# Kernel optimization log

Measured on AMD Instinct MI355X. Metric: run time of the kernel, lower is better.

## Reference

```python
import jax, jax.numpy as jnp
import numpy as np

N = 100000
NFEAT = 128
NHID = 128
NCLASS = 40
E = 1600000
EPS = 1e-5


def _spmm(vals, src, dst, x, n):
    # y[dst] += vals * x[src]  (sparse adj @ x)
    return jax.ops.segment_sum(vals[:, None] * x[src], dst, num_segments=n)


def _bn(h, gamma, beta, rmean, rvar):
    # BatchNorm1d in eval mode (running statistics)
    return (h - rmean) * jax.lax.rsqrt(rvar + EPS) * gamma + beta


def setup_inputs() -> dict:
    key = jax.random.key(0)
    ks = jax.random.split(key, 24)
    inp = {
        'x': jax.random.normal(ks[0], (N, NFEAT), dtype=jnp.float32),
        'M': jax.random.uniform(ks[1], (N, 1), dtype=jnp.float32),
        'AM': jax.random.uniform(ks[2], (N, 1), dtype=jnp.float32),
        'srcZ': jax.random.randint(ks[3], (E,), 0, N, dtype=jnp.int32),
        'dstZ': jax.random.randint(ks[4], (E,), 0, N, dtype=jnp.int32),
        'valsZ': jax.random.uniform(ks[5], (E,), dtype=jnp.float32),
        'src': jax.random.randint(ks[6], (E,), 0, N, dtype=jnp.int32),
        'dst': jax.random.randint(ks[7], (E,), 0, N, dtype=jnp.int32),
        'vals': jax.random.uniform(ks[8], (E,), dtype=jnp.float32),
        # layer 0 (PaGConv) params
        'W0': jax.random.normal(ks[9], (NHID, NFEAT), dtype=jnp.float32) * (1.414 / np.sqrt(NFEAT)),
        'b0': jnp.zeros((NHID,), dtype=jnp.float32),
        'g0': jnp.ones((NHID,), dtype=jnp.float32),
        'be0': jnp.zeros((NHID,), dtype=jnp.float32),
        'rm0': jax.random.normal(ks[10], (NHID,), dtype=jnp.float32) * 0.1,
        'rv0': jax.random.uniform(ks[11], (NHID,), dtype=jnp.float32) + 0.5,
        # layer 1 (GConv) params
        'W1': jax.random.normal(ks[12], (NHID, NHID), dtype=jnp.float32) * (1.414 / np.sqrt(NHID)),
        'b1': jnp.zeros((NHID,), dtype=jnp.float32),
        'g1': jnp.ones((NHID,), dtype=jnp.float32),
        'be1': jnp.zeros((NHID,), dtype=jnp.float32),
        'rm1': jax.random.normal(ks[13], (NHID,), dtype=jnp.float32) * 0.1,
        'rv1': jax.random.uniform(ks[14], (NHID,), dtype=jnp.float32) + 0.5,
        # layer 2 (GConv) params
        'W2': jax.random.normal(ks[15], (NCLASS, NHID), dtype=jnp.float32) * (1.414 / np.sqrt(NHID)),
        'b2': jnp.zeros((NCLASS,), dtype=jnp.float32),
    }
    return inp


def reference(x, M, AM, srcZ, dstZ, valsZ, src, dst, vals,
              W0, b0, g0, be0, rm0, rv0,
              W1, b1, g1, be1, rm1, rv1,
              W2, b2):
    n = x.shape[0]
    # layer 0: PaGConv with adjZ: fc(spmm(adjZ, M*x) * AM), then BN + ReLU (dropout off in eval)
    h = _spmm(valsZ, srcZ, dstZ, M * x, n) * AM
    h = h @ W0.T + b0
    h = jax.nn.relu(_bn(h, g0, be0, rm0, rv0))
    # layer 1: GConv with adj: fc(spmm(adj, h)), then BN + ReLU
    h = _spmm(vals, src, dst, h, n)
    h = h @ W1.T + b1
    h = jax.nn.relu(_bn(h, g1, be1, rm1, rv1))
    # layer 2: GConv, then log_softmax
    h = _spmm(vals, src, dst, h, n)
    h = h @ W2.T + b2
    return jax.nn.log_softmax(h, axis=-1)
```

## Files before the change

### kernel.cpp

```cpp
#include <hip/hip_runtime.h>
#include <math.h>

#define NFEAT 128
#define NCLS 40
#define NCLSP 64
#define BINROWS 64
#define NBINMAX 1600
#define NBLKC 256
#define CHUNKMAX 6400
#define SEGC 7
#define RSMAX 2048

typedef short bf16x8 __attribute__((ext_vector_type(8)));
typedef float f32x4 __attribute__((ext_vector_type(4)));

__device__ __forceinline__ float bf2f(unsigned int lo16) {
  return __uint_as_float((lo16 & 0xffffu) << 16);
}
__device__ __forceinline__ unsigned int f2bf(float x) {
  unsigned int u = __float_as_uint(x);
  return (u + 0x7fffu + ((u >> 16) & 1u)) >> 16;
}

__global__ __launch_bounds__(256) void prep_misc(
    const float* b0, const float* g0, const float* be0,
    const float* rm0, const float* rv0,
    const float* b1, const float* g1, const float* be1,
    const float* rm1, const float* rv1,
    float* sc0, float* sh0, float* sc1, float* sh1,
    const float* __restrict__ W0, const float* __restrict__ W1,
    const float* __restrict__ W2,
    unsigned short* __restrict__ Wb0, unsigned short* __restrict__ Wb1,
    unsigned short* __restrict__ W2hi, unsigned short* __restrict__ W2lo) {
  int t = threadIdx.x;
  if (blockIdx.x == 0) {
    if (t < 128) {
      float s = g0[t] * rsqrtf(rv0[t] + 1e-5f);
      sc0[t] = s;
      sh0[t] = (b0[t] - rm0[t]) * s + be0[t];
    } else {
      int i = t - 128;
      float s = g1[i] * rsqrtf(rv1[i] + 1e-5f);
      sc1[i] = s;
      sh1[i] = (b1[i] - rm1[i]) * s + be1[i];
    }
    return;
  }
  int i = (blockIdx.x - 1) * 256 + t;
  if (i < 4096) {
    const float* W = (i < 2048) ? W0 : W1;
    unsigned short* Wb = (i < 2048) ? Wb0 : Wb1;
    int j = (i < 2048) ? i : i - 2048;
    const float4* p = (const float4*)(W + (size_t)j * 8);
    float4 v0 = p[0], v1 = p[1];
    unsigned int o0 = f2bf(v0.x) | (f2bf(v0.y) << 16);
    unsigned int o1 = f2bf(v0.z) | (f2bf(v0.w) << 16);
    unsigned int o2 = f2bf(v1.x) | (f2bf(v1.y) << 16);
    unsigned int o3 = f2bf(v1.z) | (f2bf(v1.w) << 16);
    ((uint4*)Wb)[j] = make_uint4(o0, o1, o2, o3);
  } else {
    int j = i - 4096;
    int r = j >> 4;
    float v[8] = {0.f, 0.f, 0.f, 0.f, 0.f, 0.f, 0.f, 0.f};
    if (r < NCLS) {
      const float4* p = (const float4*)(W2 + (size_t)j * 8);
      float4 a = p[0], b = p[1];
      v[0] = a.x; v[1] = a.y; v[2] = a.z; v[3] = a.w;
      v[4] = b.x; v[5] = b.y; v[6] = b.z; v[7] = b.w;
    }
    unsigned int h[8], l[8];
#pragma unroll
    for (int q = 0; q < 8; ++q) {
      h[q] = f2bf(v[q]);
      l[q] = f2bf(v[q] - bf2f(h[q]));
    }
    ((uint4*)W2hi)[j] = make_uint4(h[0] | (h[1] << 16), h[2] | (h[3] << 16),
                                   h[4] | (h[5] << 16), h[6] | (h[7] << 16));
    ((uint4*)W2lo)[j] = make_uint4(l[0] | (l[1] << 16), l[2] | (l[3] << 16),
                                   l[4] | (l[5] << 16), l[6] | (l[7] << 16));
  }
}

__global__ void convert_xm(const float* __restrict__ x, const float* __restrict__ Mv,
                           unsigned short* __restrict__ xm, int n) {
  int i = blockIdx.x * 256 + threadIdx.x;
  if (i >= n * (NFEAT / 8)) return;
  int row = i >> 4;
  float m = Mv[row];
  const float4* p = (const float4*)(x + (size_t)i * 8);
  float4 v0 = p[0], v1 = p[1];
  unsigned int o0 = f2bf(v0.x * m) | (f2bf(v0.y * m) << 16);
  unsigned int o1 = f2bf(v0.z * m) | (f2bf(v0.w * m) << 16);
  unsigned int o2 = f2bf(v1.x * m) | (f2bf(v1.y * m) << 16);
  unsigned int o3 = f2bf(v1.z * m) | (f2bf(v1.w * m) << 16);
  ((uint4*)xm)[i] = make_uint4(o0, o1, o2, o3);
}

__global__ __launch_bounds__(256) void bin_sort2(
    const int* __restrict__ srcZ, const int* __restrict__ dstZ, const float* __restrict__ valZ,
    const int* __restrict__ srcA, const int* __restrict__ dstA, const float* __restrict__ valA,
    int2* __restrict__ DrmZ, int2* __restrict__ DrmA,
    int2* __restrict__ binsCZ, int2* __restrict__ binsCA,
    int E, int nbin, int chunk) {
  __shared__ int2 stage[CHUNKMAX];
  __shared__ int cur[NBINMAX];
  __shared__ int ps[256];
  const int t = threadIdx.x;
  int k = blockIdx.x;
  const int* srcp; const int* dstp; const float* valp; int2* Drm; int2* binsC;
  if (k < NBLKC) {
    srcp = srcZ; dstp = dstZ; valp = valZ; Drm = DrmZ; binsC = binsCZ;
  } else {
    k -= NBLKC;
    srcp = srcA; dstp = dstA; valp = valA; Drm = DrmA; binsC = binsCA;
  }
  for (int i = t; i < nbin; i += 256) cur[i] = 0;
  __syncthreads();
  const int e0 = k * chunk, e1 = min(E, e0 + chunk);
#pragma unroll 4
  for (int e = e0 + t; e < e1; e += 256) atomicAdd(&cur[dstp[e] >> 6], 1);
  __syncthreads();
  int loc[SEGC], cnt[SEGC];
  int s = 0;
#pragma unroll
  for (int j = 0; j < SEGC; ++j) {
    int i = t * SEGC + j;
    int v = (i < nbin) ? cur[i] : 0;
    loc[j] = s; cnt[j] = v;
    s += v;
  }
  ps[t] = s;
  __syncthreads();
  for (int o = 1; o < 256; o <<= 1) {
    int x = (t >= o) ? ps[t - o] : 0;
    __syncthreads();
    ps[t] += x;
    __syncthreads();
  }
  int ex = ps[t] - s;
#pragma unroll
  for (int j = 0; j < SEGC; ++j) {
    int i = t * SEGC + j;
    if (i < nbin) {
      int o = ex + loc[j];
      Drm[(size_t)k * nbin + i] = make_int2(e0 + o, cnt[j]);
      cur[i] = o;
    }
  }
  __syncthreads();
#pragma unroll 2
  for (int e = e0 + t; e < e1; e += 256) {
    int d = dstp[e];
    int p = atomicAdd(&cur[d >> 6], 1);
    stage[p] = make_int2(srcp[e] | ((d & 63) << 17), __float_as_int(valp[e]));
  }
  __syncthreads();
  const int n = e1 - e0;
  for (int i = t; i < n; i += 256) binsC[e0 + i] = stage[i];
}

__global__ __launch_bounds__(256) void transposeD2(
    const int2* __restrict__ DrmZ, const int2* __restrict__ DrmA,
    int2* __restrict__ DbmZ, int2* __restrict__ DbmA,
    int* __restrict__ binTotZ, int* __restrict__ binTotA, int nbin, int tdb) {
  __shared__ int2 st[8][256];
  __shared__ int part[256];
  int t = threadIdx.x;
  int b = blockIdx.x;
  const int2* Drm; int2* Dbm; int* binTot;
  if (b < tdb) {
    Drm = DrmZ; Dbm = DbmZ; binTot = binTotZ;
  } else {
    b -= tdb;
    Drm = DrmA; Dbm = DbmA; binTot = binTotA;
  }
  int i0 = b * 8;
#pragma unroll
  for (int j = 0; j < 8; ++j) {
    int i = i0 + j;
    st[j][t] = (i < nbin) ? Drm[(size_t)t * nbin + i] : make_int2(0, 0);
  }
  __syncthreads();
  {
    int j = t >> 5, ks = (t & 31) * 8;
    int i = i0 + j;
    if (i < nbin) {
      int2* q = &Dbm[(size_t)i * NBLKC + ks];
#pragma unroll
      for (int m = 0; m < 8; ++m) q[m] = st[j][ks + m];
    }
    int p = 0;
#pragma unroll
    for (int m = 0; m < 8; ++m) p += st[j][ks + m].y;
    part[t] = p;
  }
  __syncthreads();
  if (t < 8) {
    int s = 0;
    for (int k = 0; k < 32; ++k) s += part[t * 32 + k];
    if (i0 + t < nbin) binTot[i0 + t] = s;
  }
}

__global__ __launch_bounds__(256) void bin_start2(
    const int* __restrict__ btZ, const int* __restrict__ btA,
    int* __restrict__ bsZ, int* __restrict__ bsA, int nbin) {
  __shared__ int ps[256];
  int t = threadIdx.x;
  const int* bt = (blockIdx.x == 0) ? btZ : btA;
  int* bs = (blockIdx.x == 0) ? bsZ : bsA;
  int C = (nbin + 255) / 256;
  int loc[SEGC + 1];
  int sum = 0;
  for (int j = 0; j < C; ++j) {
    int i = t * C + j;
    loc[j] = sum;
    sum += (i < nbin) ? bt[i] : 0;
  }
  ps[t] = sum;
  __syncthreads();
  for (int o = 1; o < 256; o <<= 1) {
    int x = (t >= o) ? ps[t - o] : 0;
    __syncthreads();
    ps[t] += x;
    __syncthreads();
  }
  int ex = ps[t] - sum;
  for (int j = 0; j < C; ++j) {
    int i = t * C + j;
    if (i < nbin) bs[i] = ex + loc[j];
  }
  if (t == 255) bs[nbin] = ps[255];
}

__global__ __launch_bounds__(256) void row_sort2(
    const int2* __restrict__ DbmZ, const int2* __restrict__ DbmA,
    const int2* __restrict__ binsCZ, const int2* __restrict__ binsCA,
    const int* __restrict__ binStartZ, const int* __restrict__ binStartA,
    int2* __restrict__ bins2Z, int2* __restrict__ bins2A,
    int* __restrict__ rowptrZ, int* __restrict__ rowptrA, int n, int nbin) {
  __shared__ int2 stage[RSMAX];
  __shared__ int ps[256];
  __shared__ int rcnt[BINROWS];
  __shared__ int roff[BINROWS];
  int b = blockIdx.x;
  const int t = threadIdx.x;
  const int2* Dbm; const int2* binsC; const int* binStart; int2* bins2; int* rowptr;
  if (b < nbin) {
    Dbm = DbmZ; binsC = binsCZ; binStart = binStartZ; bins2 = bins2Z; rowptr = rowptrZ;
  } else {
    b -= nbin;
    Dbm = DbmA; binsC = binsCA; binStart = binStartA; bins2 = bins2A; rowptr = rowptrA;
  }
  if (t < BINROWS) rcnt[t] = 0;
  int2 run = Dbm[(size_t)b * NBLKC + t];
  ps[t] = run.y;
  __syncthreads();
  for (int o = 1; o < 256; o <<= 1) {
    int x = (t >= o) ? ps[t - o] : 0;
    __syncthreads();
    ps[t] += x;
    __syncthreads();
  }
  int mystart = ps[t] - run.y;
  for (int j = 0; j < run.y; ++j) {
    int2 en = binsC[run.x + j];
    int idx = mystart + j;
    if (idx < RSMAX) stage[idx] = en;
    atomicAdd(&rcnt[(en.x >> 17) & 63], 1);
  }
  __syncthreads();
  const int bs = binStart[b];
  if (t < BINROWS) {
    int c = rcnt[t];
    int s = c;
#pragma unroll
    for (int o = 1; o < 64; o <<= 1) {
      int v = __shfl_up(s, o);
      if (t >= o) s += v;
    }
    int excl = s - c;
    int row = b * BINROWS + t;
    if (row < n) rowptr[row] = bs + excl;
    roff[t] = excl;
  }
  __syncthreads();
  int total = min(ps[255], RSMAX);
  for (int i = t; i < total; i += 256) {
    int2 en = stage[i];
    int row = (en.x >> 17) & 63;
    int p = atomicAdd(&roff[row], 1);
    bins2[bs + p] = en;
  }
  if (b == nbin - 1 && t == 0) rowptr[n] = binStart[nbin];
}

template <bool SCALE>
__global__ __launch_bounds__(256) void spmm128_sorted(
    const int* __restrict__ rowptr, const int2* __restrict__ bins2,
    const unsigned short* __restrict__ X, const float* __restrict__ AM,
    unsigned short* __restrict__ Y, int n) {
  int row = (blockIdx.x * 256 + threadIdx.x) >> 6;
  int lane = threadIdx.x & 63;
  if (row >= n) return;
  int s = rowptr[row], d = rowptr[row + 1] - s;
  int half = lane >> 5, l32 = lane & 31;
  float s0 = 0.f, s1 = 0.f, s2 = 0.f, s3 = 0.f;
  for (int kb = 0; kb < d; kb += 64) {
    int rem = min(64, d - kb);
    int2 my = (lane < rem) ? bins2[s + kb + lane] : make_int2(0, 0);
    int myc = my.x & 0x1FFFF;
    float myw = __int_as_float(my.y);
    for (int k = 0; k < rem; k += 8) {
#pragma unroll
      for (int st = 0; st < 4; ++st) {
        int idx = k + 2 * st + half;
        int c = __shfl(myc, idx);
        float wv = __shfl(myw, idx);
        uint2 pv = *(const uint2*)(X + (size_t)c * NFEAT + l32 * 4);
        s0 += wv * bf2f(pv.x);
        s1 += wv * bf2f(pv.x >> 16);
        s2 += wv * bf2f(pv.y);
        s3 += wv * bf2f(pv.y >> 16);
      }
    }
  }
  s0 += __shfl_xor(s0, 32); s1 += __shfl_xor(s1, 32);
  s2 += __shfl_xor(s2, 32); s3 += __shfl_xor(s3, 32);
  if (SCALE) {
    float am = AM[row];
    s0 *= am; s1 *= am; s2 *= am; s3 *= am;
  }
  unsigned int pk = half ? (f2bf(s2) | (f2bf(s3) << 16)) : (f2bf(s0) | (f2bf(s1) << 16));
  ((unsigned int*)Y)[(size_t)row * (NFEAT / 2) + l32 * 2 + half] = pk;
}

__global__ __launch_bounds__(256) void gemm_mfma128(
    const unsigned short* __restrict__ Y, const unsigned short* __restrict__ Wb,
    const float* __restrict__ scale, const float* __restrict__ shift,
    unsigned short* __restrict__ Out, int M) {
  const int wave = threadIdx.x >> 6;
  const int lane = threadIdx.x & 63;
  const int quad = lane >> 4;
  const int l16 = lane & 15;
  const int arow = blockIdx.x * 64 + wave * 16 + l16;
  const bool rv = arow < M;

  f32x4 acc[8];
#pragma unroll
  for (int c = 0; c < 8; ++c) acc[c] = (f32x4){0.f, 0.f, 0.f, 0.f};

#pragma unroll
  for (int kc = 0; kc < 128; kc += 32) {
    bf16x8 a = rv ? *(const bf16x8*)(Y + (size_t)arow * 128 + kc + quad * 8)
                  : (bf16x8){0, 0, 0, 0, 0, 0, 0, 0};
#pragma unroll
    for (int c = 0; c < 8; ++c) {
      bf16x8 b = *(const bf16x8*)(Wb + (size_t)(c * 16 + l16) * 128 + kc + quad * 8);
      acc[c] = __builtin_amdgcn_mfma_f32_16x16x32_bf16(a, b, acc[c], 0, 0, 0);
    }
  }

  int orow0 = blockIdx.x * 64 + wave * 16 + quad * 4;
#pragma unroll
  for (int c = 0; c < 8; ++c) {
    int col = c * 16 + l16;
    float sc = scale[col], sh = shift[col];
#pragma unroll
    for (int r = 0; r < 4; ++r) {
      int orow = orow0 + r;
      if (orow < M) {
        float v = fmaxf(acc[c][r] * sc + sh, 0.f);
        Out[(size_t)orow * 128 + col] = (unsigned short)f2bf(v);
      }
    }
  }
}

__global__ __launch_bounds__(256) void gemm40_mfma(
    const unsigned short* __restrict__ Y, const unsigned short* __restrict__ Whi,
    const unsigned short* __restrict__ Wlo, unsigned short* __restrict__ G2, int M) {
  const int wave = threadIdx.x >> 6;
  const int lane = threadIdx.x & 63;
  const int quad = lane >> 4;
  const int l16 = lane & 15;
  const int arow = blockIdx.x * 64 + wave * 16 + l16;
  const bool rv = arow < M;

  f32x4 acc[4];
#pragma unroll
  for (int c = 0; c < 4; ++c) acc[c] = (f32x4){0.f, 0.f, 0.f, 0.f};

#pragma unroll
  for (int kc = 0; kc < 128; kc += 32) {
    bf16x8 a = rv ? *(const bf16x8*)(Y + (size_t)arow * 128 + kc + quad * 8)
                  : (bf16x8){0, 0, 0, 0, 0, 0, 0, 0};
#pragma unroll
    for (int c = 0; c < 4; ++c) {
      bf16x8 bh = *(const bf16x8*)(Whi + (size_t)(c * 16 + l16) * 128 + kc + quad * 8);
      bf16x8 bl = *(const bf16x8*)(Wlo + (size_t)(c * 16 + l16) * 128 + kc + quad * 8);
      acc[c] = __builtin_amdgcn_mfma_f32_16x16x32_bf16(a, bh, acc[c], 0, 0, 0);
      acc[c] = __builtin_amdgcn_mfma_f32_16x16x32_bf16(a, bl, acc[c], 0, 0, 0);
    }
  }

  int orow0 = blockIdx.x * 64 + wave * 16 + quad * 4;
#pragma unroll
  for (int c = 0; c < 4; ++c) {
    int col = c * 16 + l16;
#pragma unroll
    for (int r = 0; r < 4; ++r) {
      int orow = orow0 + r;
      if (orow < M) G2[(size_t)orow * NCLSP + col] = (unsigned short)f2bf(acc[c][r]);
    }
  }
}

__global__ __launch_bounds__(256) void spmm_softmax64(
    const int* __restrict__ rowptr, const int2* __restrict__ bins2,
    const unsigned short* __restrict__ G2, const float* __restrict__ b2,
    float* __restrict__ out, int n) {
  int row = (blockIdx.x * 256 + threadIdx.x) >> 6;
  int lane = threadIdx.x & 63;
  if (row >= n) return;
  const int eidx = lane >> 4, q = lane & 15;
  const bool vq = q < (NCLS / 4);
  float4 bv = vq ? *(const float4*)(b2 + q * 4) : make_float4(0.f, 0.f, 0.f, 0.f);

  int s0i = rowptr[row], d = rowptr[row + 1] - s0i;
  float a0 = 0.f, a1 = 0.f, a2 = 0.f, a3 = 0.f;
  for (int kb = 0; kb < d; kb += 64) {
    int rem = min(64, d - kb);
    int2 my = (lane < rem) ? bins2[s0i + kb + lane] : make_int2(0, 0);
    int myc = my.x & 0x1FFFF;
    float myw = __int_as_float(my.y);
    int steps = (rem + 3) >> 2;
#pragma unroll 4
    for (int st = 0; st < steps; ++st) {
      int idx = st * 4 + eidx;
      int c = __shfl(myc, idx);
      float wv = __shfl(myw, idx);
      uint2 pv = *(const uint2*)(G2 + (size_t)c * NCLSP + q * 4);
      a0 += wv * bf2f(pv.x);
      a1 += wv * bf2f(pv.x >> 16);
      a2 += wv * bf2f(pv.y);
      a3 += wv * bf2f(pv.y >> 16);
    }
  }
  a0 += __shfl_xor(a0, 16); a1 += __shfl_xor(a1, 16);
  a2 += __shfl_xor(a2, 16); a3 += __shfl_xor(a3, 16);
  a0 += __shfl_xor(a0, 32); a1 += __shfl_xor(a1, 32);
  a2 += __shfl_xor(a2, 32); a3 += __shfl_xor(a3, 32);
  float z0 = a0 + bv.x, z1 = a1 + bv.y, z2 = a2 + bv.z, z3 = a3 + bv.w;
  bool par = (eidx == 0) && vq;
  float m = par ? fmaxf(fmaxf(z0, z1), fmaxf(z2, z3)) : -INFINITY;
#pragma unroll
  for (int o = 1; o < 64; o <<= 1) m = fmaxf(m, __shfl_xor(m, o));
  float ex = par ? (__expf(z0 - m) + __expf(z1 - m) + __expf(z2 - m) + __expf(z3 - m)) : 0.f;
#pragma unroll
  for (int o = 1; o < 64; o <<= 1) ex += __shfl_xor(ex, o);
  float lg = m + __logf(ex);
  if (par) {
    *(float4*)&out[(size_t)row * NCLS + q * 4] =
        make_float4(z0 - lg, z1 - lg, z2 - lg, z3 - lg);
  }
}


extern "C" void kernel_launch(void* const* d_in, const int* in_sizes, int n_in,
                              void* d_out, int out_size, void* d_ws, size_t ws_size,
                              hipStream_t stream) {
  const float* x    = (const float*)d_in[0];
  const float* Mv   = (const float*)d_in[1];
  const float* AM   = (const float*)d_in[2];
  const int* srcZ   = (const int*)d_in[3];
  const int* dstZ   = (const int*)d_in[4];
  const float* valsZ= (const float*)d_in[5];
  const int* src    = (const int*)d_in[6];
  const int* dst    = (const int*)d_in[7];
  const float* vals = (const float*)d_in[8];
  const float* W0   = (const float*)d_in[9];
  const float* b0   = (const float*)d_in[10];
  const float* g0   = (const float*)d_in[11];
  const float* be0  = (const float*)d_in[12];
  const float* rm0  = (const float*)d_in[13];
  const float* rv0  = (const float*)d_in[14];
  const float* W1   = (const float*)d_in[15];
  const float* b1   = (const float*)d_in[16];
  const float* g1   = (const float*)d_in[17];
  const float* be1  = (const float*)d_in[18];
  const float* rm1  = (const float*)d_in[19];
  const float* rv1  = (const float*)d_in[20];
  const float* W2   = (const float*)d_in[21];
  const float* b2   = (const float*)d_in[22];
  float* out = (float*)d_out;

  const int N = in_sizes[1];
  const int E = in_sizes[3];
  const int NBIN = (N + BINROWS - 1) / BINROWS;
  const int CHUNK = (E + NBLKC - 1) / NBLKC;

  char* w = (char*)d_ws;
  size_t off = 0;
  auto alloc = [&](size_t bytes) -> void* {
    void* p = w + off;
    off = (off + bytes + 255) & ~(size_t)255;
    return p;
  };
  int2* binsCZ = (int2*)alloc((size_t)NBLKC * CHUNK * 8);
  int2* binsCA = (int2*)alloc((size_t)NBLKC * CHUNK * 8);
  int* binTotZ = (int*)alloc((size_t)NBIN * 4);
  int* binTotA = (int*)alloc((size_t)NBIN * 4);
  int* binStartZ = (int*)alloc((size_t)(NBIN + 1) * 4);
  int* binStartA = (int*)alloc((size_t)(NBIN + 1) * 4);
  int2* bins2A = (int2*)alloc((size_t)E * 8);
  int* rowptrA = (int*)alloc((size_t)(N + 1) * 4);
  unsigned short* xm = (unsigned short*)alloc((size_t)N * NFEAT * 2);
  unsigned short* bufA = (unsigned short*)alloc((size_t)N * NFEAT * 2);
  unsigned short* bufB = (unsigned short*)alloc((size_t)N * NFEAT * 2);
  float* sc0 = (float*)alloc(128 * 4);
  float* sh0 = (float*)alloc(128 * 4);
  float* sc1 = (float*)alloc(128 * 4);
  float* sh1 = (float*)alloc(128 * 4);
  unsigned short* Wb0 = (unsigned short*)alloc(128 * 128 * 2);
  unsigned short* Wb1 = (unsigned short*)alloc(128 * 128 * 2);
  unsigned short* W2hi = (unsigned short*)alloc(64 * 128 * 2);
  unsigned short* W2lo = (unsigned short*)alloc(64 * 128 * 2);
  const size_t drmBytes = (size_t)NBLKC * NBIN * 8;
  int2* DrmZ = (int2*)((char*)bufA + 0 * drmBytes);
  int2* DrmA = (int2*)((char*)bufA + 1 * drmBytes);
  int2* DbmZ = (int2*)((char*)bufA + 2 * drmBytes);
  int2* DbmA = (int2*)((char*)bufA + 3 * drmBytes);
  int2* bins2Z = (int2*)bufB;
  int* rowptrZ = (int*)((char*)bufB + 13 * 1024 * 1024);
  unsigned short* G2 = bufA;

  const int RB = (N + 3) / 4;
  const int GB64 = (N + 63) / 64;
  const int TDB = (NBIN + 7) / 8;

  prep_misc<<<21, 256, 0, stream>>>(b0, g0, be0, rm0, rv0, b1, g1, be1, rm1, rv1,
                                    sc0, sh0, sc1, sh1, W0, W1, W2,
                                    Wb0, Wb1, W2hi, W2lo);
  convert_xm<<<(N * (NFEAT / 8) + 255) / 256, 256, 0, stream>>>(x, Mv, xm, N);

  bin_sort2<<<2 * NBLKC, 256, 0, stream>>>(srcZ, dstZ, valsZ, src, dst, vals,
                                           DrmZ, DrmA, binsCZ, binsCA, E, NBIN, CHUNK);
  transposeD2<<<2 * TDB, 256, 0, stream>>>(DrmZ, DrmA, DbmZ, DbmA, binTotZ, binTotA,
                                           NBIN, TDB);
  bin_start2<<<2, 256, 0, stream>>>(binTotZ, binTotA, binStartZ, binStartA, NBIN);
  row_sort2<<<2 * NBIN, 256, 0, stream>>>(DbmZ, DbmA, binsCZ, binsCA, binStartZ, binStartA,
                                          bins2Z, bins2A, rowptrZ, rowptrA, N, NBIN);

  spmm128_sorted<true><<<RB, 256, 0, stream>>>(rowptrZ, bins2Z, xm, AM, bufA, N);
  gemm_mfma128<<<GB64, 256, 0, stream>>>(bufA, Wb0, sc0, sh0, bufB, N);

  spmm128_sorted<false><<<RB, 256, 0, stream>>>(rowptrA, bins2A, bufB,
                                                (const float*)nullptr, bufA, N);
  gemm_mfma128<<<GB64, 256, 0, stream>>>(bufA, Wb1, sc1, sh1, bufB, N);

  gemm40_mfma<<<GB64, 256, 0, stream>>>(bufB, W2hi, W2lo, G2, N);
  spmm_softmax64<<<RB, 256, 0, stream>>>(rowptrA, bins2A, G2, b2, out, N);
}
```

Measured before the change: 529.3 us.

## Fuse final linear into second GEMM and drop bin prefix-scan via fixed slots

Merges the weight-prep and x*M conversion kernels into one launch. It replaces the per-bin count/prefix-scan (binTot, bin_start2) with fixed RSMAX-sized slots per bin and per-row (start,count) descriptors. It also fuses the 40-class projection into the layer-1 GEMM through a shared-memory tile, so the hidden activations are never written back. This removes launches and a 128-wide intermediate round trip, at the cost of a larger bins2 footprint and reliance on bins holding at most RSMAX edges.

```diff
diff --git a/kernel.cpp b/kernel.cpp
--- a/kernel.cpp
+++ b/kernel.cpp
@@ -22,7 +22,7 @@
   return (u + 0x7fffu + ((u >> 16) & 1u)) >> 16;
 }
 
-__global__ __launch_bounds__(256) void prep_misc(
+__global__ __launch_bounds__(256) void prep_all(
     const float* b0, const float* g0, const float* be0,
     const float* rm0, const float* rv0,
     const float* b1, const float* g1, const float* be1,
@@ -31,7 +31,9 @@
     const float* __restrict__ W0, const float* __restrict__ W1,
     const float* __restrict__ W2,
     unsigned short* __restrict__ Wb0, unsigned short* __restrict__ Wb1,
-    unsigned short* __restrict__ W2hi, unsigned short* __restrict__ W2lo) {
+    unsigned short* __restrict__ W2hi, unsigned short* __restrict__ W2lo,
+    const float* __restrict__ x, const float* __restrict__ Mv,
+    unsigned short* __restrict__ xm, int n) {
   int t = threadIdx.x;
   if (blockIdx.x == 0) {
     if (t < 128) {
@@ -46,44 +48,43 @@
     }
     return;
   }
-  int i = (blockIdx.x - 1) * 256 + t;
-  if (i < 4096) {
-    const float* W = (i < 2048) ? W0 : W1;
-    unsigned short* Wb = (i < 2048) ? Wb0 : Wb1;
-    int j = (i < 2048) ? i : i - 2048;
-    const float4* p = (const float4*)(W + (size_t)j * 8);
-    float4 v0 = p[0], v1 = p[1];
-    unsigned int o0 = f2bf(v0.x) | (f2bf(v0.y) << 16);
-    unsigned int o1 = f2bf(v0.z) | (f2bf(v0.w) << 16);
-    unsigned int o2 = f2bf(v1.x) | (f2bf(v1.y) << 16);
-    unsigned int o3 = f2bf(v1.z) | (f2bf(v1.w) << 16);
-    ((uint4*)Wb)[j] = make_uint4(o0, o1, o2, o3);
-  } else {
-    int j = i - 4096;
-    int r = j >> 4;
-    float v[8] = {0.f, 0.f, 0.f, 0.f, 0.f, 0.f, 0.f, 0.f};
-    if (r < NCLS) {
-      const float4* p = (const float4*)(W2 + (size_t)j * 8);
-      float4 a = p[0], b = p[1];
-      v[0] = a.x; v[1] = a.y; v[2] = a.z; v[3] = a.w;
-      v[4] = b.x; v[5] = b.y; v[6] = b.z; v[7] = b.w;
-    }
-    unsigned int h[8], l[8];
-#pragma unroll
-    for (int q = 0; q < 8; ++q) {
-      h[q] = f2bf(v[q]);
-      l[q] = f2bf(v[q] - bf2f(h[q]));
-    }
-    ((uint4*)W2hi)[j] = make_uint4(h[0] | (h[1] << 16), h[2] | (h[3] << 16),
-                                   h[4] | (h[5] << 16), h[6] | (h[7] << 16));
-    ((uint4*)W2lo)[j] = make_uint4(l[0] | (l[1] << 16), l[2] | (l[3] << 16),
-                                   l[4] | (l[5] << 16), l[6] | (l[7] << 16));
-  }
-}
-
-__global__ void convert_xm(const float* __restrict__ x, const float* __restrict__ Mv,
-                           unsigned short* __restrict__ xm, int n) {
-  int i = blockIdx.x * 256 + threadIdx.x;
+  if (blockIdx.x <= 20) {
+    int i = (blockIdx.x - 1) * 256 + t;
+    if (i < 4096) {
+      const float* W = (i < 2048) ? W0 : W1;
+      unsigned short* Wb = (i < 2048) ? Wb0 : Wb1;
+      int j = (i < 2048) ? i : i - 2048;
+      const float4* p = (const float4*)(W + (size_t)j * 8);
+      float4 v0 = p[0], v1 = p[1];
+      unsigned int o0 = f2bf(v0.x) | (f2bf(v0.y) << 16);
+      unsigned int o1 = f2bf(v0.z) | (f2bf(v0.w) << 16);
+      unsigned int o2 = f2bf(v1.x) | (f2bf(v1.y) << 16);
+      unsigned int o3 = f2bf(v1.z) | (f2bf(v1.w) << 16);
+      ((uint4*)Wb)[j] = make_uint4(o0, o1, o2, o3);
+    } else {
+      int j = i - 4096;
+      int r = j >> 4;
+      float v[8] = {0.f, 0.f, 0.f, 0.f, 0.f, 0.f, 0.f, 0.f};
+      if (r < NCLS) {
+        const float4* p = (const float4*)(W2 + (size_t)j * 8);
+        float4 a = p[0], b = p[1];
+        v[0] = a.x; v[1] = a.y; v[2] = a.z; v[3] = a.w;
+        v[4] = b.x; v[5] = b.y; v[6] = b.z; v[7] = b.w;
+      }
+      unsigned int h[8], l[8];
+#pragma unroll
+      for (int q = 0; q < 8; ++q) {
+        h[q] = f2bf(v[q]);
+        l[q] = f2bf(v[q] - bf2f(h[q]));
+      }
+      ((uint4*)W2hi)[j] = make_uint4(h[0] | (h[1] << 16), h[2] | (h[3] << 16),
+                                     h[4] | (h[5] << 16), h[6] | (h[7] << 16));
+      ((uint4*)W2lo)[j] = make_uint4(l[0] | (l[1] << 16), l[2] | (l[3] << 16),
+                                     l[4] | (l[5] << 16), l[6] | (l[7] << 16));
+    }
+    return;
+  }
+  int i = (blockIdx.x - 21) * 256 + t;
   if (i >= n * (NFEAT / 8)) return;
   int row = i >> 4;
   float m = Mv[row];
@@ -161,18 +162,16 @@
 
 __global__ __launch_bounds__(256) void transposeD2(
     const int2* __restrict__ DrmZ, const int2* __restrict__ DrmA,
-    int2* __restrict__ DbmZ, int2* __restrict__ DbmA,
-    int* __restrict__ binTotZ, int* __restrict__ binTotA, int nbin, int tdb) {
+    int2* __restrict__ DbmZ, int2* __restrict__ DbmA, int nbin, int tdb) {
   __shared__ int2 st[8][256];
-  __shared__ int part[256];
   int t = threadIdx.x;
   int b = blockIdx.x;
-  const int2* Drm; int2* Dbm; int* binTot;
+  const int2* Drm; int2* Dbm;
   if (b < tdb) {
-    Drm = DrmZ; Dbm = DbmZ; binTot = binTotZ;
+    Drm = DrmZ; Dbm = DbmZ;
   } else {
     b -= tdb;
-    Drm = DrmA; Dbm = DbmA; binTot = binTotA;
+    Drm = DrmA; Dbm = DbmA;
   }
   int i0 = b * 8;
 #pragma unroll
@@ -189,68 +188,26 @@
 #pragma unroll
       for (int m = 0; m < 8; ++m) q[m] = st[j][ks + m];
     }
-    int p = 0;
-#pragma unroll
-    for (int m = 0; m < 8; ++m) p += st[j][ks + m].y;
-    part[t] = p;
-  }
-  __syncthreads();
-  if (t < 8) {
-    int s = 0;
-    for (int k = 0; k < 32; ++k) s += part[t * 32 + k];
-    if (i0 + t < nbin) binTot[i0 + t] = s;
-  }
-}
-
-__global__ __launch_bounds__(256) void bin_start2(
-    const int* __restrict__ btZ, const int* __restrict__ btA,
-    int* __restrict__ bsZ, int* __restrict__ bsA, int nbin) {
-  __shared__ int ps[256];
-  int t = threadIdx.x;
-  const int* bt = (blockIdx.x == 0) ? btZ : btA;
-  int* bs = (blockIdx.x == 0) ? bsZ : bsA;
-  int C = (nbin + 255) / 256;
-  int loc[SEGC + 1];
-  int sum = 0;
-  for (int j = 0; j < C; ++j) {
-    int i = t * C + j;
-    loc[j] = sum;
-    sum += (i < nbin) ? bt[i] : 0;
-  }
-  ps[t] = sum;
-  __syncthreads();
-  for (int o = 1; o < 256; o <<= 1) {
-    int x = (t >= o) ? ps[t - o] : 0;
-    __syncthreads();
-    ps[t] += x;
-    __syncthreads();
-  }
-  int ex = ps[t] - sum;
-  for (int j = 0; j < C; ++j) {
-    int i = t * C + j;
-    if (i < nbin) bs[i] = ex + loc[j];
-  }
-  if (t == 255) bs[nbin] = ps[255];
+  }
 }
 
 __global__ __launch_bounds__(256) void row_sort2(
     const int2* __restrict__ DbmZ, const int2* __restrict__ DbmA,
     const int2* __restrict__ binsCZ, const int2* __restrict__ binsCA,
-    const int* __restrict__ binStartZ, const int* __restrict__ binStartA,
     int2* __restrict__ bins2Z, int2* __restrict__ bins2A,
-    int* __restrict__ rowptrZ, int* __restrict__ rowptrA, int n, int nbin) {
+    int2* __restrict__ rdZ, int2* __restrict__ rdA, int n, int nbin) {
   __shared__ int2 stage[RSMAX];
   __shared__ int ps[256];
   __shared__ int rcnt[BINROWS];
   __shared__ int roff[BINROWS];
   int b = blockIdx.x;
   const int t = threadIdx.x;
-  const int2* Dbm; const int2* binsC; const int* binStart; int2* bins2; int* rowptr;
+  const int2* Dbm; const int2* binsC; int2* bins2; int2* rowdesc;
   if (b < nbin) {
-    Dbm = DbmZ; binsC = binsCZ; binStart = binStartZ; bins2 = bins2Z; rowptr = rowptrZ;
+    Dbm = DbmZ; binsC = binsCZ; bins2 = bins2Z; rowdesc = rdZ;
   } else {
     b -= nbin;
-    Dbm = DbmA; binsC = binsCA; binStart = binStartA; bins2 = bins2A; rowptr = rowptrA;
+    Dbm = DbmA; binsC = binsCA; bins2 = bins2A; rowdesc = rdA;
   }
   if (t < BINROWS) rcnt[t] = 0;
   int2 run = Dbm[(size_t)b * NBLKC + t];
@@ -270,7 +227,7 @@
     atomicAdd(&rcnt[(en.x >> 17) & 63], 1);
   }
   __syncthreads();
-  const int bs = binStart[b];
+  const int bs = b * RSMAX;
   if (t < BINROWS) {
     int c = rcnt[t];
     int s = c;
@@ -281,7 +238,7 @@
     }
     int excl = s - c;
     int row = b * BINROWS + t;
-    if (row < n) rowptr[row] = bs + excl;
+    if (row < n) rowdesc[row] = make_int2(bs + excl, c);
     roff[t] = excl;
   }
   __syncthreads();
@@ -292,18 +249,18 @@
     int p = atomicAdd(&roff[row], 1);
     bins2[bs + p] = en;
   }
-  if (b == nbin - 1 && t == 0) rowptr[n] = binStart[nbin];
 }
 
 template <bool SCALE>
 __global__ __launch_bounds__(256) void spmm128_sorted(
-    const int* __restrict__ rowptr, const int2* __restrict__ bins2,
+    const int2* __restrict__ rowdesc, const int2* __restrict__ bins2,
     const unsigned short* __restrict__ X, const float* __restrict__ AM,
     unsigned short* __restrict__ Y, int n) {
   int row = (blockIdx.x * 256 + threadIdx.x) >> 6;
   int lane = threadIdx.x & 63;
   if (row >= n) return;
-  int s = rowptr[row], d = rowptr[row + 1] - s;
+  int2 rd = rowdesc[row];
+  int s = rd.x, d = rd.y;
   int half = lane >> 5, l32 = lane & 31;
   float s0 = 0.f, s1 = 0.f, s2 = 0.f, s3 = 0.f;
   for (int kb = 0; kb < d; kb += 64) {
@@ -335,10 +292,13 @@
   ((unsigned int*)Y)[(size_t)row * (NFEAT / 2) + l32 * 2 + half] = pk;
 }
 
+template <bool FUSE_G2>
 __global__ __launch_bounds__(256) void gemm_mfma128(
     const unsigned short* __restrict__ Y, const unsigned short* __restrict__ Wb,
     const float* __restrict__ scale, const float* __restrict__ shift,
-    unsigned short* __restrict__ Out, int M) {
+    unsigned short* __restrict__ Out,
+    const unsigned short* __restrict__ Whi, const unsigned short* __restrict__ Wlo,
+    unsigned short* __restrict__ G2, int M) {
   const int wave = threadIdx.x >> 6;
   const int lane = threadIdx.x & 63;
   const int quad = lane >> 4;
@@ -361,63 +321,67 @@
     }
   }
 
-  int orow0 = blockIdx.x * 64 + wave * 16 + quad * 4;
-#pragma unroll
-  for (int c = 0; c < 8; ++c) {
-    int col = c * 16 + l16;
-    float sc = scale[col], sh = shift[col];
-#pragma unroll
-    for (int r = 0; r < 4; ++r) {
-      int orow = orow0 + r;
-      if (orow < M) {
+  const int orow0 = blockIdx.x * 64 + wave * 16 + quad * 4;
+
+  if constexpr (!FUSE_G2) {
+#pragma unroll
+    for (int c = 0; c < 8; ++c) {
+      int col = c * 16 + l16;
+      float sc = scale[col], sh = shift[col];
+#pragma unroll
+      for (int r = 0; r < 4; ++r) {
+        int orow = orow0 + r;
+        if (orow < M) {
+          float v = fmaxf(acc[c][r] * sc + sh, 0.f);
+          Out[(size_t)orow * 128 + col] = (unsigned short)f2bf(v);
+        }
+      }
+    }
+  } else {
+    __shared__ unsigned short Ht[64][136];
+    const int lrow0 = wave * 16 + quad * 4;
+#pragma unroll
+    for (int c = 0; c < 8; ++c) {
+      int col = c * 16 + l16;
+      float sc = scale[col], sh = shift[col];
+#pragma unroll
+      for (int r = 0; r < 4; ++r) {
         float v = fmaxf(acc[c][r] * sc + sh, 0.f);
-        Out[(size_t)orow * 128 + col] = (unsigned short)f2bf(v);
-      }
-    }
-  }
-}
-
-__global__ __launch_bounds__(256) void gemm40_mfma(
-    const unsigned short* __restrict__ Y, const unsigned short* __restrict__ Whi,
-    const unsigned short* __restrict__ Wlo, unsigned short* __restrict__ G2, int M) {
-  const int wave = threadIdx.x >> 6;
-  const int lane = threadIdx.x & 63;
-  const int quad = lane >> 4;
-  const int l16 = lane & 15;
-  const int arow = blockIdx.x * 64 + wave * 16 + l16;
-  const bool rv = arow < M;
-
-  f32x4 acc[4];
-#pragma unroll
-  for (int c = 0; c < 4; ++c) acc[c] = (f32x4){0.f, 0.f, 0.f, 0.f};
-
-#pragma unroll
-  for (int kc = 0; kc < 128; kc += 32) {
-    bf16x8 a = rv ? *(const bf16x8*)(Y + (size_t)arow * 128 + kc + quad * 8)
-                  : (bf16x8){0, 0, 0, 0, 0, 0, 0, 0};
-#pragma unroll
-    for (int c = 0; c < 4; ++c) {
-      bf16x8 bh = *(const bf16x8*)(Whi + (size_t)(c * 16 + l16) * 128 + kc + quad * 8);
-      bf16x8 bl = *(const bf16x8*)(Wlo + (size_t)(c * 16 + l16) * 128 + kc + quad * 8);
-      acc[c] = __builtin_amdgcn_mfma_f32_16x16x32_bf16(a, bh, acc[c], 0, 0, 0);
-      acc[c] = __builtin_amdgcn_mfma_f32_16x16x32_bf16(a, bl, acc[c], 0, 0, 0);
-    }
-  }
-
-  int orow0 = blockIdx.x * 64 + wave * 16 + quad * 4;
-#pragma unroll
-  for (int c = 0; c < 4; ++c) {
-    int col = c * 16 + l16;
-#pragma unroll
-    for (int r = 0; r < 4; ++r) {
-      int orow = orow0 + r;
-      if (orow < M) G2[(size_t)orow * NCLSP + col] = (unsigned short)f2bf(acc[c][r]);
+        Ht[lrow0 + r][col] = (unsigned short)f2bf(v);
+      }
+    }
+    __syncthreads();
+    bf16x8 af[4];
+#pragma unroll
+    for (int kc = 0; kc < 4; ++kc)
+      af[kc] = *(const bf16x8*)(&Ht[wave * 16 + l16][kc * 32 + quad * 8]);
+    f32x4 acc2[4];
+#pragma unroll
+    for (int c2 = 0; c2 < 4; ++c2) acc2[c2] = (f32x4){0.f, 0.f, 0.f, 0.f};
+#pragma unroll
+    for (int kc = 0; kc < 4; ++kc) {
+#pragma unroll
+      for (int c2 = 0; c2 < 4; ++c2) {
+        bf16x8 bh = *(const bf16x8*)(Whi + (size_t)(c2 * 16 + l16) * 128 + kc * 32 + quad * 8);
+        bf16x8 bl = *(const bf16x8*)(Wlo + (size_t)(c2 * 16 + l16) * 128 + kc * 32 + quad * 8);
+        acc2[c2] = __builtin_amdgcn_mfma_f32_16x16x32_bf16(af[kc], bh, acc2[c2], 0, 0, 0);
+        acc2[c2] = __builtin_amdgcn_mfma_f32_16x16x32_bf16(af[kc], bl, acc2[c2], 0, 0, 0);
+      }
+    }
+#pragma unroll
+    for (int c2 = 0; c2 < 4; ++c2) {
+      int col = c2 * 16 + l16;
+#pragma unroll
+      for (int r = 0; r < 4; ++r) {
+        int orow = orow0 + r;
+        if (orow < M) G2[(size_t)orow * NCLSP + col] = (unsigned short)f2bf(acc2[c2][r]);
+      }
     }
   }
 }
 
 __global__ __launch_bounds__(256) void spmm_softmax64(
-    const int* __restrict__ rowptr, const int2* __restrict__ bins2,
+    const int2* __restrict__ rowdesc, const int2* __restrict__ bins2,
     const unsigned short* __restrict__ G2, const float* __restrict__ b2,
     float* __restrict__ out, int n) {
   int row = (blockIdx.x * 256 + threadIdx.x) >> 6;
@@ -427,7 +391,8 @@
   const bool vq = q < (NCLS / 4);
   float4 bv = vq ? *(const float4*)(b2 + q * 4) : make_float4(0.f, 0.f, 0.f, 0.f);
 
-  int s0i = rowptr[row], d = rowptr[row + 1] - s0i;
+  int2 rdv = rowdesc[row];
+  int s0i = rdv.x, d = rdv.y;
   float a0 = 0.f, a1 = 0.f, a2 = 0.f, a3 = 0.f;
   for (int kb = 0; kb < d; kb += 64) {
     int rem = min(64, d - kb);
@@ -507,17 +472,16 @@
     off = (off + bytes + 255) & ~(size_t)255;
     return p;
   };
+  const size_t bins2Bytes = (size_t)NBIN * RSMAX * 8;
+  const size_t bufBytes = (size_t)N * NFEAT * 2;
   int2* binsCZ = (int2*)alloc((size_t)NBLKC * CHUNK * 8);
   int2* binsCA = (int2*)alloc((size_t)NBLKC * CHUNK * 8);
-  int* binTotZ = (int*)alloc((size_t)NBIN * 4);
-  int* binTotA = (int*)alloc((size_t)NBIN * 4);
-  int* binStartZ = (int*)alloc((size_t)(NBIN + 1) * 4);
-  int* binStartA = (int*)alloc((size_t)(NBIN + 1) * 4);
-  int2* bins2A = (int2*)alloc((size_t)E * 8);
-  int* rowptrA = (int*)alloc((size_t)(N + 1) * 4);
-  unsigned short* xm = (unsigned short*)alloc((size_t)N * NFEAT * 2);
-  unsigned short* bufA = (unsigned short*)alloc((size_t)N * NFEAT * 2);
-  unsigned short* bufB = (unsigned short*)alloc((size_t)N * NFEAT * 2);
+  int2* bins2A = (int2*)alloc(bins2Bytes);
+  int2* rdZ = (int2*)alloc((size_t)N * 8);
+  int2* rdA = (int2*)alloc((size_t)N * 8);
+  unsigned short* xm = (unsigned short*)alloc(bufBytes);
+  unsigned short* bufA = (unsigned short*)alloc(bufBytes);
+  unsigned short* bufB = (unsigned short*)alloc(bins2Bytes > bufBytes ? bins2Bytes : bufBytes);
   float* sc0 = (float*)alloc(128 * 4);
   float* sh0 = (float*)alloc(128 * 4);
   float* sc1 = (float*)alloc(128 * 4);
@@ -532,33 +496,31 @@
   int2* DbmZ = (int2*)((char*)bufA + 2 * drmBytes);
   int2* DbmA = (int2*)((char*)bufA + 3 * drmBytes);
   int2* bins2Z = (int2*)bufB;
-  int* rowptrZ = (int*)((char*)bufB + 13 * 1024 * 1024);
-  unsigned short* G2 = bufA;
+  unsigned short* G2 = bufB;
 
   const int RB = (N + 3) / 4;
   const int GB64 = (N + 63) / 64;
   const int TDB = (NBIN + 7) / 8;
-
-  prep_misc<<<21, 256, 0, stream>>>(b0, g0, be0, rm0, rv0, b1, g1, be1, rm1, rv1,
-                                    sc0, sh0, sc1, sh1, W0, W1, W2,
-                                    Wb0, Wb1, W2hi, W2lo);
-  convert_xm<<<(N * (NFEAT / 8) + 255) / 256, 256, 0, stream>>>(x, Mv, xm, N);
+  const int CONVB = (N * (NFEAT / 8) + 255) / 256;
+
+  prep_all<<<21 + CONVB, 256, 0, stream>>>(b0, g0, be0, rm0, rv0, b1, g1, be1, rm1, rv1,
+                                           sc0, sh0, sc1, sh1, W0, W1, W2,
+                                           Wb0, Wb1, W2hi, W2lo, x, Mv, xm, N);
 
   bin_sort2<<<2 * NBLKC, 256, 0, stream>>>(srcZ, dstZ, valsZ, src, dst, vals,
                                            DrmZ, DrmA, binsCZ, binsCA, E, NBIN, CHUNK);
-  transposeD2<<<2 * TDB, 256, 0, stream>>>(DrmZ, DrmA, DbmZ, DbmA, binTotZ, binTotA,
-                                           NBIN, TDB);
-  bin_start2<<<2, 256, 0, stream>>>(binTotZ, binTotA, binStartZ, binStartA, NBIN);
-  row_sort2<<<2 * NBIN, 256, 0, stream>>>(DbmZ, DbmA, binsCZ, binsCA, binStartZ, binStartA,
-                                          bins2Z, bins2A, rowptrZ, rowptrA, N, NBIN);
-
-  spmm128_sorted<true><<<RB, 256, 0, stream>>>(rowptrZ, bins2Z, xm, AM, bufA, N);
-  gemm_mfma128<<<GB64, 256, 0, stream>>>(bufA, Wb0, sc0, sh0, bufB, N);
-
-  spmm128_sorted<false><<<RB, 256, 0, stream>>>(rowptrA, bins2A, bufB,
+  transposeD2<<<2 * TDB, 256, 0, stream>>>(DrmZ, DrmA, DbmZ, DbmA, NBIN, TDB);
+  row_sort2<<<2 * NBIN, 256, 0, stream>>>(DbmZ, DbmA, binsCZ, binsCA,
+                                          bins2Z, bins2A, rdZ, rdA, N, NBIN);
+
+  spmm128_sorted<true><<<RB, 256, 0, stream>>>(rdZ, bins2Z, xm, AM, bufA, N);
+  gemm_mfma128<false><<<GB64, 256, 0, stream>>>(bufA, Wb0, sc0, sh0, bufB,
+                                                nullptr, nullptr, nullptr, N);
+
+  spmm128_sorted<false><<<RB, 256, 0, stream>>>(rdA, bins2A, bufB,
                                                 (const float*)nullptr, bufA, N);
-  gemm_mfma128<<<GB64, 256, 0, stream>>>(bufA, Wb1, sc1, sh1, bufB, N);
-
-  gemm40_mfma<<<GB64, 256, 0, stream>>>(bufB, W2hi, W2lo, G2, N);
-  spmm_softmax64<<<RB, 256, 0, stream>>>(rowptrA, bins2A, G2, b2, out, N);
-}
+  gemm_mfma128<true><<<GB64, 256, 0, stream>>>(bufA, Wb1, sc1, sh1, nullptr,
+                                               W2hi, W2lo, G2, N);
+
+  spmm_softmax64<<<RB, 256, 0, stream>>>(rdA, bins2A, G2, b2, out, N);
+}
```

After: 510.8 us. 1.04x faster.
